# Optimization experiments

Measured on AMD Instinct MI355X. Metric: run time of the kernel, lower is better.

## Reference

```python
import jax, jax.numpy as jnp
import numpy as np

D_MODEL = 1024
H = 16
D_K = D_MODEL // H
B = 2
S = 2048


def setup_inputs() -> dict:
    key = jax.random.key(0)
    ks = jax.random.split(key, 11)
    scale = 1.0 / np.sqrt(D_MODEL)
    inp = {
        "query": jax.random.normal(ks[0], (B, S, D_MODEL), jnp.float32),
        "key_in": jax.random.normal(ks[1], (B, S, D_MODEL), jnp.float32),
        "value": jax.random.normal(ks[2], (B, S, D_MODEL), jnp.float32),
        # causal mask, broadcast over heads: 1 = keep, 0 = masked
        "mask": jnp.tril(jnp.ones((S, S), jnp.int32))[None, None, :, :].repeat(B, axis=0),
        "w_q": jax.random.normal(ks[3], (D_MODEL, D_MODEL), jnp.float32) * scale,
        "b_q": jax.random.normal(ks[4], (D_MODEL,), jnp.float32) * 0.01,
        "w_k": jax.random.normal(ks[5], (D_MODEL, D_MODEL), jnp.float32) * scale,
        "b_k": jax.random.normal(ks[6], (D_MODEL,), jnp.float32) * 0.01,
        "w_v": jax.random.normal(ks[7], (D_MODEL, D_MODEL), jnp.float32) * scale,
        "b_v": jax.random.normal(ks[8], (D_MODEL,), jnp.float32) * 0.01,
        "w_out": jax.random.normal(ks[9], (D_MODEL, D_MODEL), jnp.float32) * scale,
        "b_out": jax.random.normal(ks[10], (D_MODEL,), jnp.float32) * 0.01,
    }
    return inp


def _split_heads(x):
    # [B,S,D] -> [B,H,S,d_k]
    b, s, _ = x.shape
    return x.reshape(b, s, H, D_K).transpose(0, 2, 1, 3)


def reference(query, key_in, value, mask, w_q, b_q, w_k, b_k, w_v, b_v, w_out, b_out):
    q = _split_heads(query @ w_q.T + b_q)
    k = _split_heads(key_in @ w_k.T + b_k)
    v = _split_heads(value @ w_v.T + b_v)
    scores = jnp.einsum("bhqd,bhkd->bhqk", q, k) / jnp.sqrt(jnp.float32(D_K))
    scores = jnp.where(mask == 0, jnp.float32(-1e9), scores)
    attn = jax.nn.softmax(scores, axis=-1)  # dropout rate 0.0 -> identity
    out = jnp.einsum("bhqk,bhkd->bhqd", attn, v)
    out = out.transpose(0, 2, 1, 3).reshape(query.shape[0], -1, D_MODEL)
    return out @ w_out.T + b_out
```

## Files before the change

kernel.cpp:

```cpp
#include <hip/hip_runtime.h>
#include <hip/hip_bf16.h>
#include <type_traits>

#define D_MODEL 1024
#define NH 16
#define DKH 64
#define BB 2
#define SS 2048
#define MTOT (BB * SS)

typedef __hip_bfloat16 bf16;
typedef __attribute__((ext_vector_type(8))) short short8;
typedef __attribute__((ext_vector_type(4))) short short4v;
typedef __attribute__((ext_vector_type(4))) float floatx4;

__device__ __forceinline__ bf16 f2bf(float x) { return __float2bfloat16(x); }

__device__ __forceinline__ void async_cp16(const void* g, void* l) {
  __builtin_amdgcn_global_load_lds(
      (const __attribute__((address_space(1))) unsigned int*)g,
      (__attribute__((address_space(3))) unsigned int*)l, 16, 0, 0);
}

__global__ __launch_bounds__(256) void convert_w_kernel(
    const float* __restrict__ wq, const float* __restrict__ wk,
    const float* __restrict__ wv, const float* __restrict__ wo,
    bf16* __restrict__ out) {
  const int id = blockIdx.x * 256 + threadIdx.x;
  const int m = id >> 18;
  const int loc = id & 262143;
  const float* src = (m == 0) ? wq : (m == 1) ? wk : (m == 2) ? wv : wo;
  const float4 v = *(const float4*)(src + (size_t)loc * 4);
  short4v s;
  bf16* pb = (bf16*)&s;
  pb[0] = f2bf(v.x); pb[1] = f2bf(v.y); pb[2] = f2bf(v.z); pb[3] = f2bf(v.w);
  *(short4v*)(out + ((size_t)m << 20) + (size_t)loc * 4) = s;
}

__device__ __forceinline__ void gemm_qkv_body(const float* __restrict__ A,
                                              const bf16* __restrict__ W,
                                              const float* __restrict__ Bi,
                                              bf16* __restrict__ C, int mode) {
  constexpr int N = 1024, K = 1024;
  __shared__ float As[2][128 * 32];
  __shared__ bf16 Ws[2][128 * 32];

  const int tid = threadIdx.x;
  const int w = tid >> 6, lane = tid & 63, quad = lane >> 4, n16 = lane & 15;
  const int bx = blockIdx.x;
  const int bm = bx & 31, bn = bx >> 5;
  const int wm = (w & 1) * 64, wn = (w >> 1) * 64;

  const int rf = lane >> 3, cf = lane & 7;
  const int rb = lane >> 2, cb = lane & 3;

  const float* Ag0 = A + (size_t)(bm * 128) * K;
  const bf16* Wg0 = W + (size_t)(bn * 128) * K;

  auto issue = [&](int buf, int k0) {
#pragma unroll
    for (int ii = 0; ii < 4; ii++) {
      const int R = w * 32 + ii * 8 + rf;
      async_cp16(Ag0 + (size_t)R * K + k0 + ((cf ^ (R & 7)) * 4),
                 (void*)&As[buf][(w * 32 + ii * 8) * 32]);
    }
#pragma unroll
    for (int ii = 0; ii < 2; ii++) {
      const int R = w * 32 + ii * 16 + rb;
      async_cp16(Wg0 + (size_t)R * K + k0 + cb * 8,
                 (void*)&Ws[buf][(w * 32 + ii * 16) * 32]);
    }
  };

  floatx4 acc[4][4] = {};
  issue(0, 0);
  int buf = 0;
  for (int k0 = 0; k0 < K; k0 += 32) {
    __syncthreads();
    if (k0 + 32 < K) issue(buf ^ 1, k0 + 32);

    short8 af[4], bfr[4];
#pragma unroll
    for (int i = 0; i < 4; i++) {
      const int Rr = wm + i * 16 + n16;
      const float* ap = &As[buf][Rr * 32];
      const float4 f0 = *(const float4*)(ap + (((quad * 2 + 0) ^ (Rr & 7)) * 4));
      const float4 f1 = *(const float4*)(ap + (((quad * 2 + 1) ^ (Rr & 7)) * 4));
      bf16* pb = (bf16*)&af[i];
      pb[0] = f2bf(f0.x); pb[1] = f2bf(f0.y); pb[2] = f2bf(f0.z); pb[3] = f2bf(f0.w);
      pb[4] = f2bf(f1.x); pb[5] = f2bf(f1.y); pb[6] = f2bf(f1.z); pb[7] = f2bf(f1.w);
    }
#pragma unroll
    for (int j = 0; j < 4; j++)
      bfr[j] = *(const short8*)(&Ws[buf][(wn + j * 16 + n16) * 32 + quad * 8]);
#pragma unroll
    for (int i = 0; i < 4; i++)
#pragma unroll
      for (int j = 0; j < 4; j++)
        acc[i][j] = __builtin_amdgcn_mfma_f32_16x16x32_bf16(af[i], bfr[j], acc[i][j], 0, 0, 0);
    buf ^= 1;
  }

  float bv[4];
#pragma unroll
  for (int j = 0; j < 4; j++) bv[j] = Bi[bn * 128 + wn + j * 16 + n16];

#pragma unroll
  for (int i = 0; i < 4; i++) {
    const int rowb = bm * 128 + wm + i * 16 + quad * 4;
#pragma unroll
    for (int j = 0; j < 4; j++) {
      const int col = bn * 128 + wn + j * 16 + n16;
      if (mode == 1) {
        short4v s;
        bf16* pb = (bf16*)&s;
#pragma unroll
        for (int r = 0; r < 4; r++) pb[r] = f2bf(acc[i][j][r] + bv[j]);
        *(short4v*)(C + (size_t)col * MTOT + rowb) = s;
      } else {
#pragma unroll
        for (int r = 0; r < 4; r++)
          C[(size_t)(rowb + r) * N + col] = f2bf(acc[i][j][r] + bv[j]);
      }
    }
  }
}

__global__ __launch_bounds__(256) void gemm_qkv_kernel(
    const float* __restrict__ q_in, const float* __restrict__ k_in,
    const float* __restrict__ v_in, const bf16* __restrict__ Wb,
    const float* __restrict__ bq, const float* __restrict__ bk,
    const float* __restrict__ bv, bf16* __restrict__ Qw,
    bf16* __restrict__ Kw, bf16* __restrict__ VTw) {
  const int z = blockIdx.z;
  const float* A = (z == 0) ? q_in : (z == 1) ? k_in : v_in;
  const bf16* W = Wb + ((size_t)z << 20);
  const float* Bi = (z == 0) ? bq : (z == 1) ? bk : bv;
  bf16* C = (z == 0) ? Qw : (z == 1) ? Kw : VTw;
  gemm_qkv_body(A, W, Bi, C, (z == 2) ? 1 : 0);
}

__global__ __launch_bounds__(256) void gemm_out_kernel(
    const bf16* __restrict__ A, const bf16* __restrict__ W,
    const float* __restrict__ Bi, float* __restrict__ C) {
  constexpr int N = 1024, K = 1024;
  __shared__ bf16 As[2][64 * 32];
  __shared__ bf16 Ws[2][128 * 32];

  const int tid = threadIdx.x;
  const int w = tid >> 6, lane = tid & 63, quad = lane >> 4, n16 = lane & 15;
  const int bx = blockIdx.x;
  const int bm = bx & 63, bn = bx >> 6;
  const int wm = (w & 1) * 32, wn = (w >> 1) * 64;

  const int rl = lane >> 2, cl = lane & 3;

  const bf16* Ag0 = A + (size_t)(bm * 64) * K;
  const bf16* Wg0 = W + (size_t)(bn * 128) * K;

  auto issue = [&](int buf, int kk) {
    async_cp16(Ag0 + (size_t)(w * 16 + rl) * K + kk + cl * 8,
               (void*)&As[buf][(w * 16) * 32]);
    const bf16* Wg = Wg0 + kk;
#pragma unroll
    for (int ii = 0; ii < 2; ii++) {
      const int R = w * 32 + ii * 16 + rl;
      async_cp16(Wg + (size_t)R * K + cl * 8,
                 (void*)&Ws[buf][(w * 32 + ii * 16) * 32]);
    }
  };

  floatx4 acc[2][4] = {};
  issue(0, 0);
  int buf = 0;
  for (int k0 = 0; k0 < K; k0 += 32) {
    __syncthreads();
    if (k0 + 32 < K) issue(buf ^ 1, k0 + 32);

    short8 af[2], bfr[4];
#pragma unroll
    for (int i = 0; i < 2; i++)
      af[i] = *(const short8*)(&As[buf][(wm + i * 16 + n16) * 32 + quad * 8]);
#pragma unroll
    for (int j = 0; j < 4; j++)
      bfr[j] = *(const short8*)(&Ws[buf][(wn + j * 16 + n16) * 32 + quad * 8]);
#pragma unroll
    for (int i = 0; i < 2; i++)
#pragma unroll
      for (int j = 0; j < 4; j++)
        acc[i][j] = __builtin_amdgcn_mfma_f32_16x16x32_bf16(af[i], bfr[j], acc[i][j], 0, 0, 0);
    buf ^= 1;
  }

  float bv[4];
#pragma unroll
  for (int j = 0; j < 4; j++) bv[j] = Bi[bn * 128 + wn + j * 16 + n16];

#pragma unroll
  for (int i = 0; i < 2; i++) {
    const int rowb = bm * 64 + wm + i * 16 + quad * 4;
#pragma unroll
    for (int j = 0; j < 4; j++) {
      const int col = bn * 128 + wn + j * 16 + n16;
#pragma unroll
      for (int r = 0; r < 4; r++)
        C[(size_t)(rowb + r) * N + col] = acc[i][j][r] + bv[j];
    }
  }
}

__global__ __launch_bounds__(256) void attn_kernel(const bf16* __restrict__ Q,
                                                   const bf16* __restrict__ Kg,
                                                   const bf16* __restrict__ VT,
                                                   bf16* __restrict__ O) {
  constexpr int BN = 128, LDK = 72, LDV = 136, LDP = 136;
  __shared__ bf16 Ks[128 * LDK];
  __shared__ bf16 Vs[64 * LDV];
  __shared__ bf16 Pw[4 * 16 * LDP];

  const int tid = threadIdx.x;
  const int w = tid >> 6, lane = tid & 63, quad = lane >> 4, n16 = lane & 15;
  const int hb = blockIdx.x;
  const int h = hb & 15, b = hb >> 4, p = blockIdx.y;
  const size_t qoff = (size_t)b * SS * D_MODEL + h * DKH;
  const bf16* VTh = VT + (size_t)(h * DKH) * MTOT + (size_t)b * SS;

  const int kvr = tid >> 3, ck = tid & 7;
  const int dd = tid >> 4, cv = tid & 15;

  short8 kreg[4], vreg[4];
  auto loadKV = [&](int kv0) {
#pragma unroll
    for (int ii = 0; ii < 4; ii++) {
      kreg[ii] = *(const short8*)(Kg + qoff + (size_t)(kv0 + ii * 32 + kvr) * D_MODEL + ck * 8);
      vreg[ii] = *(const short8*)(VTh + (size_t)(ii * 16 + dd) * MTOT + kv0 + cv * 8);
    }
  };

  for (int hf = 0; hf < 2; hf++) {
    const int q0 = (hf == 0) ? p * 64 : (31 - p) * 64;
    const int q0w = q0 + w * 16;
    const int nt = (q0 + 191) >> 7;

    short8 aQ0, aQ1;
    {
      const bf16* qp = Q + qoff + (size_t)(q0w + n16) * D_MODEL + quad * 8;
      aQ0 = *(const short8*)(qp);
      aQ1 = *(const short8*)(qp + 32);
    }

    floatx4 facc[4] = {};
    float l_p[4] = {0.f, 0.f, 0.f, 0.f};

    loadKV(0);
    for (int t = 0; t < nt; t++) {
#pragma unroll
      for (int ii = 0; ii < 4; ii++) {
        *(short8*)(&Ks[(ii * 32 + kvr) * LDK + ck * 8]) = kreg[ii];
        *(short8*)(&Vs[(ii * 16 + dd) * LDV + cv * 8]) = vreg[ii];
      }
      __syncthreads();
      if (t + 1 < nt) loadKV((t + 1) * BN);

      const int kv0 = t * BN;
      const bool lastT = (t == nt - 1);
      float pv[8][4];
      const int qrow_base = q0w + quad * 4;
#pragma unroll
      for (int blk = 0; blk < 8; blk++) {
        floatx4 z = {};
        short8 bk0 = *(const short8*)(&Ks[(blk * 16 + n16) * LDK + quad * 8]);
        short8 bk1 = *(const short8*)(&Ks[(blk * 16 + n16) * LDK + 32 + quad * 8]);
        z = __builtin_amdgcn_mfma_f32_16x16x32_bf16(aQ0, bk0, z, 0, 0, 0);
        z = __builtin_amdgcn_mfma_f32_16x16x32_bf16(aQ1, bk1, z, 0, 0, 0);
        if (lastT) {
          const int kvg = kv0 + blk * 16 + n16;
#pragma unroll
          for (int r = 0; r < 4; r++) {
            float pe = __expf(z[r] * 0.125f);
            if (kvg > qrow_base + r) pe = 0.f;
            pv[blk][r] = pe;
            l_p[r] += pe;
          }
        } else {
#pragma unroll
          for (int r = 0; r < 4; r++) {
            const float pe = __expf(z[r] * 0.125f);
            pv[blk][r] = pe;
            l_p[r] += pe;
          }
        }
      }

      bf16* pw = &Pw[w * 16 * LDP];
#pragma unroll
      for (int blk = 0; blk < 8; blk++)
#pragma unroll
        for (int r = 0; r < 4; r++)
          pw[(quad * 4 + r) * LDP + blk * 16 + n16] = f2bf(pv[blk][r]);

      short8 aP[4];
#pragma unroll
      for (int c = 0; c < 4; c++)
        aP[c] = *(const short8*)(&pw[n16 * LDP + c * 32 + quad * 8]);

#pragma unroll
      for (int d = 0; d < 4; d++)
#pragma unroll
        for (int c = 0; c < 4; c++) {
          short8 bvf = *(const short8*)(&Vs[(d * 16 + n16) * LDV + c * 32 + quad * 8]);
          facc[d] = __builtin_amdgcn_mfma_f32_16x16x32_bf16(aP[c], bvf, facc[d], 0, 0, 0);
        }
      __syncthreads();
    }

#pragma unroll
    for (int off = 1; off < 16; off <<= 1)
#pragma unroll
      for (int r = 0; r < 4; r++) l_p[r] += __shfl_xor(l_p[r], off, 64);

#pragma unroll
    for (int r = 0; r < 4; r++) {
      const float inv = 1.f / l_p[r];
      const int qrow = q0w + quad * 4 + r;
      bf16* op = O + qoff + (size_t)qrow * D_MODEL;
#pragma unroll
      for (int d = 0; d < 4; d++) op[d * 16 + n16] = f2bf(facc[d][r] * inv);
    }
  }
}

extern "C" void kernel_launch(void* const* d_in, const int* in_sizes, int n_in,
                              void* d_out, int out_size, void* d_ws, size_t ws_size,
                              hipStream_t stream) {
  (void)in_sizes; (void)n_in; (void)out_size; (void)ws_size;
  const float* query  = (const float*)d_in[0];
  const float* key_in = (const float*)d_in[1];
  const float* value  = (const float*)d_in[2];
  const float* w_q = (const float*)d_in[4];
  const float* b_q = (const float*)d_in[5];
  const float* w_k = (const float*)d_in[6];
  const float* b_k = (const float*)d_in[7];
  const float* w_v = (const float*)d_in[8];
  const float* b_v = (const float*)d_in[9];
  const float* w_o = (const float*)d_in[10];
  const float* b_o = (const float*)d_in[11];
  float* outp = (float*)d_out;

  const size_t mat = (size_t)MTOT * D_MODEL;
  bf16* Qws  = (bf16*)d_ws;
  bf16* Kws  = Qws + mat;
  bf16* VTws = Kws + mat;
  bf16* Wb   = VTws + mat;

  convert_w_kernel<<<4096, 256, 0, stream>>>(w_q, w_k, w_v, w_o, Wb);

  dim3 gq(256, 1, 3);
  gemm_qkv_kernel<<<gq, 256, 0, stream>>>(query, key_in, value, Wb, b_q, b_k,
                                          b_v, Qws, Kws, VTws);
  dim3 ga(NH * BB, 16);
  attn_kernel<<<ga, 256, 0, stream>>>(Qws, Kws, VTws, Qws);
  gemm_out_kernel<<<512, 256, 0, stream>>>(Qws, Wb + ((size_t)3 << 20), b_o, outp);
}
```

Baseline: 254.3 us.

## Pre-convert activations to bf16 and retile the output projection GEMM

Extends the weight conversion kernel to also convert the query/key/value activations to bf16, storing two of them in the output buffer as scratch. The QKV GEMM then streams bf16 A tiles directly into LDS, halving A load bytes and removing per-iteration fp32-to-bf16 conversion. The output GEMM switches to 64x64 tiles with twice as many blocks, trading reuse for occupancy. Adds an extra conversion pass over the activations and relies on workspace/output buffer space for scratch.

New measurement: 242.9 us. -4.5%, faster.

```diff
diff --git a/kernel.cpp b/kernel.cpp
--- a/kernel.cpp
+++ b/kernel.cpp
@@ -1,6 +1,5 @@
 #include <hip/hip_runtime.h>
 #include <hip/hip_bf16.h>
-#include <type_traits>
 
 #define D_MODEL 1024
 #define NH 16
@@ -22,27 +21,38 @@
       (__attribute__((address_space(3))) unsigned int*)l, 16, 0, 0);
 }
 
-__global__ __launch_bounds__(256) void convert_w_kernel(
+__global__ __launch_bounds__(256) void convert_kernel(
     const float* __restrict__ wq, const float* __restrict__ wk,
     const float* __restrict__ wv, const float* __restrict__ wo,
-    bf16* __restrict__ out) {
+    const float* __restrict__ qi, const float* __restrict__ ki,
+    const float* __restrict__ vi, bf16* __restrict__ Wb,
+    bf16* __restrict__ Qi, bf16* __restrict__ Ki, bf16* __restrict__ Vi) {
   const int id = blockIdx.x * 256 + threadIdx.x;
-  const int m = id >> 18;
-  const int loc = id & 262143;
-  const float* src = (m == 0) ? wq : (m == 1) ? wk : (m == 2) ? wv : wo;
-  const float4 v = *(const float4*)(src + (size_t)loc * 4);
+  const float* src;
+  bf16* dst;
+  if (id < (1 << 20)) {
+    const int m = id >> 18, loc = id & 0x3FFFF;
+    src = ((m == 0) ? wq : (m == 1) ? wk : (m == 2) ? wv : wo) + (size_t)loc * 4;
+    dst = Wb + ((size_t)m << 20) + (size_t)loc * 4;
+  } else {
+    const int t = id - (1 << 20);
+    const int m = t >> 20, loc = t & 0xFFFFF;
+    src = ((m == 0) ? qi : (m == 1) ? ki : vi) + (size_t)loc * 4;
+    dst = ((m == 0) ? Qi : (m == 1) ? Ki : Vi) + (size_t)loc * 4;
+  }
+  const float4 v = *(const float4*)src;
   short4v s;
   bf16* pb = (bf16*)&s;
   pb[0] = f2bf(v.x); pb[1] = f2bf(v.y); pb[2] = f2bf(v.z); pb[3] = f2bf(v.w);
-  *(short4v*)(out + ((size_t)m << 20) + (size_t)loc * 4) = s;
-}
-
-__device__ __forceinline__ void gemm_qkv_body(const float* __restrict__ A,
+  *(short4v*)dst = s;
+}
+
+__device__ __forceinline__ void gemm_qkv_body(const bf16* __restrict__ A,
                                               const bf16* __restrict__ W,
                                               const float* __restrict__ Bi,
                                               bf16* __restrict__ C, int mode) {
   constexpr int N = 1024, K = 1024;
-  __shared__ float As[2][128 * 32];
+  __shared__ bf16 As[2][128 * 32];
   __shared__ bf16 Ws[2][128 * 32];
 
   const int tid = threadIdx.x;
@@ -51,22 +61,17 @@
   const int bm = bx & 31, bn = bx >> 5;
   const int wm = (w & 1) * 64, wn = (w >> 1) * 64;
 
-  const int rf = lane >> 3, cf = lane & 7;
   const int rb = lane >> 2, cb = lane & 3;
 
-  const float* Ag0 = A + (size_t)(bm * 128) * K;
+  const bf16* Ag0 = A + (size_t)(bm * 128) * K;
   const bf16* Wg0 = W + (size_t)(bn * 128) * K;
 
   auto issue = [&](int buf, int k0) {
-#pragma unroll
-    for (int ii = 0; ii < 4; ii++) {
-      const int R = w * 32 + ii * 8 + rf;
-      async_cp16(Ag0 + (size_t)R * K + k0 + ((cf ^ (R & 7)) * 4),
-                 (void*)&As[buf][(w * 32 + ii * 8) * 32]);
-    }
 #pragma unroll
     for (int ii = 0; ii < 2; ii++) {
       const int R = w * 32 + ii * 16 + rb;
+      async_cp16(Ag0 + (size_t)R * K + k0 + cb * 8,
+                 (void*)&As[buf][(w * 32 + ii * 16) * 32]);
       async_cp16(Wg0 + (size_t)R * K + k0 + cb * 8,
                  (void*)&Ws[buf][(w * 32 + ii * 16) * 32]);
     }
@@ -81,15 +86,8 @@
 
     short8 af[4], bfr[4];
 #pragma unroll
-    for (int i = 0; i < 4; i++) {
-      const int Rr = wm + i * 16 + n16;
-      const float* ap = &As[buf][Rr * 32];
-      const float4 f0 = *(const float4*)(ap + (((quad * 2 + 0) ^ (Rr & 7)) * 4));
-      const float4 f1 = *(const float4*)(ap + (((quad * 2 + 1) ^ (Rr & 7)) * 4));
-      bf16* pb = (bf16*)&af[i];
-      pb[0] = f2bf(f0.x); pb[1] = f2bf(f0.y); pb[2] = f2bf(f0.z); pb[3] = f2bf(f0.w);
-      pb[4] = f2bf(f1.x); pb[5] = f2bf(f1.y); pb[6] = f2bf(f1.z); pb[7] = f2bf(f1.w);
-    }
+    for (int i = 0; i < 4; i++)
+      af[i] = *(const short8*)(&As[buf][(wm + i * 16 + n16) * 32 + quad * 8]);
 #pragma unroll
     for (int j = 0; j < 4; j++)
       bfr[j] = *(const short8*)(&Ws[buf][(wn + j * 16 + n16) * 32 + quad * 8]);
@@ -127,13 +125,13 @@
 }
 
 __global__ __launch_bounds__(256) void gemm_qkv_kernel(
-    const float* __restrict__ q_in, const float* __restrict__ k_in,
-    const float* __restrict__ v_in, const bf16* __restrict__ Wb,
+    const bf16* __restrict__ Qi, const bf16* __restrict__ Ki,
+    const bf16* __restrict__ Vi, const bf16* __restrict__ Wb,
     const float* __restrict__ bq, const float* __restrict__ bk,
     const float* __restrict__ bv, bf16* __restrict__ Qw,
     bf16* __restrict__ Kw, bf16* __restrict__ VTw) {
   const int z = blockIdx.z;
-  const float* A = (z == 0) ? q_in : (z == 1) ? k_in : v_in;
+  const bf16* A = (z == 0) ? Qi : (z == 1) ? Ki : Vi;
   const bf16* W = Wb + ((size_t)z << 20);
   const float* Bi = (z == 0) ? bq : (z == 1) ? bk : bv;
   bf16* C = (z == 0) ? Qw : (z == 1) ? Kw : VTw;
@@ -145,67 +143,52 @@
     const float* __restrict__ Bi, float* __restrict__ C) {
   constexpr int N = 1024, K = 1024;
   __shared__ bf16 As[2][64 * 32];
-  __shared__ bf16 Ws[2][128 * 32];
+  __shared__ bf16 Ws[2][64 * 32];
 
   const int tid = threadIdx.x;
   const int w = tid >> 6, lane = tid & 63, quad = lane >> 4, n16 = lane & 15;
   const int bx = blockIdx.x;
   const int bm = bx & 63, bn = bx >> 6;
-  const int wm = (w & 1) * 32, wn = (w >> 1) * 64;
-
-  const int rl = lane >> 2, cl = lane & 3;
+  const int wm = w * 16;
+
+  const int rb = lane >> 2, cb = lane & 3;
 
   const bf16* Ag0 = A + (size_t)(bm * 64) * K;
-  const bf16* Wg0 = W + (size_t)(bn * 128) * K;
+  const bf16* Wg0 = W + (size_t)(bn * 64) * K;
 
   auto issue = [&](int buf, int kk) {
-    async_cp16(Ag0 + (size_t)(w * 16 + rl) * K + kk + cl * 8,
-               (void*)&As[buf][(w * 16) * 32]);
-    const bf16* Wg = Wg0 + kk;
-#pragma unroll
-    for (int ii = 0; ii < 2; ii++) {
-      const int R = w * 32 + ii * 16 + rl;
-      async_cp16(Wg + (size_t)R * K + cl * 8,
-                 (void*)&Ws[buf][(w * 32 + ii * 16) * 32]);
-    }
+    const int R = w * 16 + rb;
+    async_cp16(Ag0 + (size_t)R * K + kk + cb * 8, (void*)&As[buf][(w * 16) * 32]);
+    async_cp16(Wg0 + (size_t)R * K + kk + cb * 8, (void*)&Ws[buf][(w * 16) * 32]);
   };
 
-  floatx4 acc[2][4] = {};
+  floatx4 acc[4] = {};
   issue(0, 0);
   int buf = 0;
   for (int k0 = 0; k0 < K; k0 += 32) {
     __syncthreads();
     if (k0 + 32 < K) issue(buf ^ 1, k0 + 32);
 
-    short8 af[2], bfr[4];
-#pragma unroll
-    for (int i = 0; i < 2; i++)
-      af[i] = *(const short8*)(&As[buf][(wm + i * 16 + n16) * 32 + quad * 8]);
-#pragma unroll
-    for (int j = 0; j < 4; j++)
-      bfr[j] = *(const short8*)(&Ws[buf][(wn + j * 16 + n16) * 32 + quad * 8]);
-#pragma unroll
-    for (int i = 0; i < 2; i++)
-#pragma unroll
-      for (int j = 0; j < 4; j++)
-        acc[i][j] = __builtin_amdgcn_mfma_f32_16x16x32_bf16(af[i], bfr[j], acc[i][j], 0, 0, 0);
+    short8 af = *(const short8*)(&As[buf][(wm + n16) * 32 + quad * 8]);
+#pragma unroll
+    for (int j = 0; j < 4; j++) {
+      short8 bfr = *(const short8*)(&Ws[buf][(j * 16 + n16) * 32 + quad * 8]);
+      acc[j] = __builtin_amdgcn_mfma_f32_16x16x32_bf16(af, bfr, acc[j], 0, 0, 0);
+    }
     buf ^= 1;
   }
 
   float bv[4];
 #pragma unroll
-  for (int j = 0; j < 4; j++) bv[j] = Bi[bn * 128 + wn + j * 16 + n16];
-
-#pragma unroll
-  for (int i = 0; i < 2; i++) {
-    const int rowb = bm * 64 + wm + i * 16 + quad * 4;
-#pragma unroll
-    for (int j = 0; j < 4; j++) {
-      const int col = bn * 128 + wn + j * 16 + n16;
-#pragma unroll
-      for (int r = 0; r < 4; r++)
-        C[(size_t)(rowb + r) * N + col] = acc[i][j][r] + bv[j];
-    }
+  for (int j = 0; j < 4; j++) bv[j] = Bi[bn * 64 + j * 16 + n16];
+
+  const int rowb = bm * 64 + wm + quad * 4;
+#pragma unroll
+  for (int j = 0; j < 4; j++) {
+    const int col = bn * 64 + j * 16 + n16;
+#pragma unroll
+    for (int r = 0; r < 4; r++)
+      C[(size_t)(rowb + r) * N + col] = acc[j][r] + bv[j];
   }
 }
 
@@ -352,13 +335,17 @@
   bf16* Kws  = Qws + mat;
   bf16* VTws = Kws + mat;
   bf16* Wb   = VTws + mat;
-
-  convert_w_kernel<<<4096, 256, 0, stream>>>(w_q, w_k, w_v, w_o, Wb);
+  bf16* Vi   = Wb + 4 * (size_t)(1 << 20);
+  bf16* Qi = (bf16*)d_out;
+  bf16* Ki = Qi + mat;
+
+  convert_kernel<<<16384, 256, 0, stream>>>(w_q, w_k, w_v, w_o, query, key_in,
+                                            value, Wb, Qi, Ki, Vi);
 
   dim3 gq(256, 1, 3);
-  gemm_qkv_kernel<<<gq, 256, 0, stream>>>(query, key_in, value, Wb, b_q, b_k,
-                                          b_v, Qws, Kws, VTws);
+  gemm_qkv_kernel<<<gq, 256, 0, stream>>>(Qi, Ki, Vi, Wb, b_q, b_k, b_v, Qws,
+                                          Kws, VTws);
   dim3 ga(NH * BB, 16);
   attn_kernel<<<ga, 256, 0, stream>>>(Qws, Kws, VTws, Qws);
-  gemm_out_kernel<<<512, 256, 0, stream>>>(Qws, Wb + ((size_t)3 << 20), b_o, outp);
-}
+  gemm_out_kernel<<<1024, 256, 0, stream>>>(Qws, Wb + ((size_t)3 << 20), b_o, outp);
+}
```
